# Optimization experiments

Hardware: AMD Instinct MI355X
Metric: run time of the kernel (lower is better)

## Reference

```python
import jax, jax.numpy as jnp
import numpy as np

P = 3            # patch size
PAD = P // 2
K = 8            # candidates kept per pixel
N_ITERS = 5
T = 1.0


def _patch_cost(qpad, kpad, sy, sx, yg, xg):
    # qpad: [C,H+2P,W+2P]; kpad: [C,Hk+2P,Wk+2P]; sy,sx: [N,H,W] int -> cost [N,H,W]
    cost = jnp.zeros(sy.shape, qpad.dtype)
    for dy in range(P):
        for dx in range(P):
            qv = qpad[:, yg + dy, xg + dx]          # [C,H,W]
            kv = kpad[:, sy + dy, sx + dx]          # [C,N,H,W]
            cost = cost + jnp.sum((qv[:, None] - kv) ** 2, axis=0)
    return cost


def _topk_merge(costs, sy, sx, k):
    # keep k smallest costs along candidate axis 0 (sorted ascending)
    neg, idx = jax.lax.top_k(jnp.moveaxis(-costs, 0, -1), k)   # [H,W,k]
    take = lambda a: jnp.moveaxis(jnp.take_along_axis(jnp.moveaxis(a, 0, -1), idx, axis=-1), -1, 0)
    return -jnp.moveaxis(neg, -1, 0), take(sy), take(sx)


def _patchmatch(q, kf, key):
    # q: [C,H,W], kf: [C,Hk,Wk] -> shift maps sy, sx: [K,H,W] int
    C, H, W = q.shape
    Hk, Wk = kf.shape[1], kf.shape[2]
    qpad = jnp.pad(q, ((0, 0), (PAD, PAD), (PAD, PAD)))
    kpad = jnp.pad(kf, ((0, 0), (PAD, PAD), (PAD, PAD)))
    yg, xg = jnp.meshgrid(jnp.arange(H), jnp.arange(W), indexing="ij")
    # random init of K candidates per pixel
    sy = jax.random.randint(jax.random.fold_in(key, 10_000), (K, H, W), 0, Hk)
    sx = jax.random.randint(jax.random.fold_in(key, 10_001), (K, H, W), 0, Wk)
    cost = _patch_cost(qpad, kpad, sy, sx, yg, xg)
    cost, sy, sx = _topk_merge(cost, sy, sx, K)
    r0 = max(Hk, Wk) // 2
    for it in range(N_ITERS):
        by, bx = sy[0], sx[0]
        # parallel propagation from 4 neighbors (shift adjusted by offset)
        cy = [jnp.roll(by, 1, 1), jnp.roll(by, -1, 1),
              jnp.roll(by, 1, 0) + 1, jnp.roll(by, -1, 0) - 1]
        cx = [jnp.roll(bx, 1, 1) + 1, jnp.roll(bx, -1, 1) - 1,
              jnp.roll(bx, 1, 0), jnp.roll(bx, -1, 0)]
        # random search around current best with shrinking radius
        kit = jax.random.fold_in(key, it)
        for s in range(2):
            rad = max(1, r0 >> s)
            dy = jax.random.randint(jax.random.fold_in(kit, 2 * s), (H, W), -rad, rad + 1)
            dx = jax.random.randint(jax.random.fold_in(kit, 2 * s + 1), (H, W), -rad, rad + 1)
            cy.append(by + dy)
            cx.append(bx + dx)
        nsy = jnp.clip(jnp.stack(cy), 0, Hk - 1)
        nsx = jnp.clip(jnp.stack(cx), 0, Wk - 1)
        ncost = _patch_cost(qpad, kpad, nsy, nsx, yg, xg)
        cost, sy, sx = _topk_merge(jnp.concatenate([cost, ncost]),
                                   jnp.concatenate([sy, nsy]),
                                   jnp.concatenate([sx, nsx]), K)
    return sy, sx


def _attention_layer(qi, ki, vi, key):
    # shifts are integer constants (search is non-differentiable in original)
    sy, sx = _patchmatch(jax.lax.stop_gradient(qi), jax.lax.stop_gradient(ki), key)
    H, W = qi.shape[1], qi.shape[2]
    yg, xg = jnp.meshgrid(jnp.arange(H), jnp.arange(W), indexing="ij")
    qpad = jnp.pad(qi, ((0, 0), (PAD, PAD), (PAD, PAD)))
    kpad = jnp.pad(ki, ((0, 0), (PAD, PAD), (PAD, PAD)))
    cost = _patch_cost(qpad, kpad, sy, sx, yg, xg)       # [K,H,W]
    w = jax.nn.softmax(-cost / T, axis=0)                # [K,H,W]
    vg = vi[:, sy, sx]                                   # [Cv,K,H,W]
    return jnp.sum(w[None] * vg, axis=1)                 # [Cv,H,W]


def setup_inputs() -> dict:
    key = jax.random.key(0)
    kq, kk, kv = jax.random.split(key, 3)
    q = jax.random.normal(kq, (2, 32, 256, 256), dtype=jnp.float32)
    k = jax.random.normal(kk, (2, 32, 256, 256), dtype=jnp.float32)
    v = jax.random.normal(kv, (2, 64, 256, 256), dtype=jnp.float32)
    return {"q": q, "k": k, "v": v}


def reference(q, k, v) -> jnp.ndarray:
    B = q.shape[0]
    keys = jax.random.split(jax.random.key(42), B)
    return jax.vmap(_attention_layer)(q, k, v, keys)     # [B,Cv,H,W]
```

## Files before the change

### kernel.cpp

```cpp
#include <hip/hip_runtime.h>
#include <stdint.h>

#define HW 256
#define HWP 258
#define CH 32
#define CVN 64
#define NPIX (HW*HW)
#define KK 8
#define CSTRT (HWP*HWP)


__host__ __device__ __forceinline__ void tf2x32(uint32_t k0, uint32_t k1,
                                                uint32_t x0, uint32_t x1,
                                                uint32_t &o0, uint32_t &o1) {
  const uint32_t ks2 = k0 ^ k1 ^ 0x1BD11BDAu;
  x0 += k0; x1 += k1;
#define TFR(r) x0 += x1; x1 = (x1 << (r)) | (x1 >> (32 - (r))); x1 ^= x0;
  TFR(13) TFR(15) TFR(26) TFR(6)
  x0 += k1;  x1 += ks2 + 1u;
  TFR(17) TFR(29) TFR(16) TFR(24)
  x0 += ks2; x1 += k0 + 2u;
  TFR(13) TFR(15) TFR(26) TFR(6)
  x0 += k0;  x1 += k1 + 3u;
  TFR(17) TFR(29) TFR(16) TFR(24)
  x0 += k1;  x1 += ks2 + 4u;
  TFR(13) TFR(15) TFR(26) TFR(6)
  x0 += ks2; x1 += k0 + 5u;
#undef TFR
  o0 = x0; o1 = x1;
}

__device__ __forceinline__ uint32_t tfbits(uint32_t k0, uint32_t k1, uint32_t idx) {
  uint32_t a, b;
  tf2x32(k0, k1, 0u, idx, a, b);
  return a ^ b;
}

__global__ __launch_bounds__(256) void tpad_k(const float* __restrict__ src,
                                              float* __restrict__ dst) {
  __shared__ float tile[CH][65];
  int t = blockIdx.x;
  int b = t >> 10;
  int p0 = (t & 1023) * 64;
  int tid = threadIdx.x;
  const float* sb = src + (size_t)b * CH * NPIX;
#pragma unroll
  for (int i = 0; i < 8; i++) {
    int idx = i * 256 + tid;
    int c = idx >> 6, px = idx & 63;
    tile[c][px] = sb[c * NPIX + p0 + px];
  }
  __syncthreads();
  float* db = dst + (size_t)b * CSTRT * CH;
#pragma unroll
  for (int i = 0; i < 8; i++) {
    int idx = i * 256 + tid;
    int px = idx >> 5, c = idx & 31;
    int p = p0 + px;
    int y = p >> 8, x = p & 255;
    db[((size_t)(y + 1) * HWP + (x + 1)) * CH + c] = tile[c][px];
  }
}

__global__ __launch_bounds__(256) void vtr_k(const float* __restrict__ v,
                                             float* __restrict__ vp) {
  __shared__ float tile[CVN][65];
  int t = blockIdx.x;
  int b = t >> 10;
  int p0 = (t & 1023) * 64;
  int tid = threadIdx.x;
  const float* sb = v + (size_t)b * CVN * NPIX;
#pragma unroll
  for (int i = 0; i < 16; i++) {
    int idx = i * 256 + tid;
    int c = idx >> 6, px = idx & 63;
    tile[c][px] = sb[c * NPIX + p0 + px];
  }
  __syncthreads();
  float* db = vp + (size_t)b * NPIX * CVN;
#pragma unroll
  for (int i = 0; i < 16; i++) {
    int idx = i * 256 + tid;
    int px = idx >> 6, c = idx & 63;
    db[(size_t)(p0 + px) * CVN + c] = tile[c][px];
  }
}

__device__ __forceinline__ float cost_full(const float* __restrict__ qt,
                                           int py, int px,
                                           const float* __restrict__ kb2,
                                           int sy, int sx) {
#pragma clang fp contract(off)
  float S[3][3];
  const float* kb = kb2 + ((size_t)sy * HWP + sx) * CH;
#pragma unroll
  for (int dy = 0; dy < 3; dy++) {
#pragma unroll
    for (int dx = 0; dx < 3; dx++) {
      int row = py + dy, col = px + dx;
      const float* qrow = &qt[(row * 18 + col) * 32];
      int rot = 4 * ((row * 3 + col) & 7);
      const float* kr = kb + (dy * HWP + dx) * CH;
      float4 kv[8], qv[8];
#pragma unroll
      for (int i = 0; i < 8; i++) kv[i] = ((const float4*)kr)[i];
#pragma unroll
      for (int i = 0; i < 8; i++)
        qv[i] = *(const float4*)(&qrow[(i * 4 + rot) & 31]);
      float s = 0.f;
#pragma unroll
      for (int i = 0; i < 8; i++) {
        float d;
        d = qv[i].x - kv[i].x; s = s + d * d;
        d = qv[i].y - kv[i].y; s = s + d * d;
        d = qv[i].z - kv[i].z; s = s + d * d;
        d = qv[i].w - kv[i].w; s = s + d * d;
      }
      S[dy][dx] = s;
    }
  }
  float cost = 0.f;
#pragma unroll
  for (int dy = 0; dy < 3; dy++)
#pragma unroll
    for (int dx = 0; dx < 3; dx++) cost = cost + S[dy][dx];
  return cost;
}

__device__ __forceinline__ float cost_ch(const float* __restrict__ qt,
                                         int py, int px,
                                         const float* __restrict__ kb2,
                                         int sy, int sx) {
#pragma clang fp contract(off)
  float S[3][3];
#pragma unroll
  for (int dy = 0; dy < 3; dy++)
#pragma unroll
    for (int dx = 0; dx < 3; dx++) S[dy][dx] = 0.f;
  const float* kb = kb2 + ((size_t)sy * HWP + sx) * CH;
#pragma unroll 2
  for (int ch = 0; ch < CH; ch += 4) {
#pragma unroll
    for (int dy = 0; dy < 3; dy++) {
#pragma unroll
      for (int dx = 0; dx < 3; dx++) {
        int row = py + dy, col = px + dx;
        const float4 qv = *(const float4*)(&qt[(row * 18 + col) * 32 +
                                              ((ch + 4 * ((row * 3 + col) & 7)) & 31)]);
        const float4 kv = *(const float4*)(kb + (dy * HWP + dx) * CH + ch);
        float d;
        d = qv.x - kv.x; S[dy][dx] = S[dy][dx] + d * d;
        d = qv.y - kv.y; S[dy][dx] = S[dy][dx] + d * d;
        d = qv.z - kv.z; S[dy][dx] = S[dy][dx] + d * d;
        d = qv.w - kv.w; S[dy][dx] = S[dy][dx] + d * d;
      }
    }
  }
  float cost = 0.f;
#pragma unroll
  for (int dy = 0; dy < 3; dy++)
#pragma unroll
    for (int dx = 0; dx < 3; dx++) cost = cost + S[dy][dx];
  return cost;
}

__device__ __forceinline__ void load_qtile16(const float* __restrict__ qpb,
                                             float* __restrict__ qt,
                                             int ty, int tx, int tid) {
  for (int i = tid; i < 18 * 18 * 8; i += 256) {
    int c4 = i & 7;
    int col = (i >> 3) % 18;
    int row = (i >> 3) / 18;
    float4 v = *(const float4*)(qpb + ((size_t)(ty + row) * HWP + (tx + col)) * CH + c4 * 4);
    *(float4*)(&qt[(row * 18 + col) * 32 +
                   ((c4 * 4 + 4 * ((row * 3 + col) & 7)) & 31)]) = v;
  }
}

__global__ __launch_bounds__(256) void init11_k(
    const float* __restrict__ qp2, const float* __restrict__ kp2,
    float* __restrict__ cO, int* __restrict__ sO,
    uint4 ikA, uint4 ikB) {
  __shared__ float qt[18 * 18 * 32];
  __shared__ uint32_t ent[2048];
  __shared__ float lc[256][9];
  __shared__ int bcnt[8], bstart[9], boff[8];
  int tid = threadIdx.x;
  int grp = blockIdx.x;
  int b = grp >> 8;
  int tin = grp & 255;
  int ty = (tin >> 4) * 16, tx = (tin & 15) * 16;
  const float* qpb = qp2 + (size_t)b * CSTRT * CH;
  const float* kpb = kp2 + (size_t)b * CSTRT * CH;
  load_qtile16(qpb, qt, ty, tx, tid);
  if (tid < 8) bcnt[tid] = 0;
  __syncthreads();

  int py = tid >> 4, px = tid & 15;
  int p = ((ty + py) << 8) | (tx + px);
  uint4 K = b ? ikB : ikA;
  int scand[KK];
#pragma unroll
  for (int j = 0; j < KK; j++) {
    uint32_t cand = (uint32_t)(j * NPIX + p);
    int sy = (int)(tfbits(K.x, K.y, cand) & 255u);
    int sx = (int)(tfbits(K.z, K.w, cand) & 255u);
    scand[j] = (sy << 8) | sx;
    atomicAdd(&bcnt[sy >> 5], 1);
  }
  __syncthreads();
  if (tid == 0) {
    int s = 0;
#pragma unroll
    for (int i = 0; i < 8; i++) { bstart[i] = s; boff[i] = s; s += bcnt[i]; }
    bstart[8] = s;
  }
  __syncthreads();
#pragma unroll
  for (int j = 0; j < KK; j++) {
    int pos = atomicAdd(&boff[scand[j] >> 13], 1);
    ent[pos] = ((uint32_t)scand[j] << 11) | ((uint32_t)tid << 3) | (uint32_t)j;
  }
  __syncthreads();

  for (int band = 0; band < 8; band++) {
    int s = bstart[band], t = bstart[band + 1];
    for (int i = s + tid; i < t; i += 256) {
      uint32_t en = ent[i];
      int j = en & 7, owner = (en >> 3) & 255;
      int ps = en >> 11;
      lc[owner][j] = cost_full(qt, owner >> 4, owner & 15, kpb, ps >> 8, ps & 255);
    }
    __syncthreads();
  }

  float c8[KK];
  int s8[KK];
#pragma unroll
  for (int jj = 0; jj < KK; jj++) { c8[jj] = lc[tid][jj]; s8[jj] = scand[jj]; }
#pragma unroll
  for (int ph = 0; ph < KK; ph++) {
#pragma unroll
    for (int i = (ph & 1); i + 1 < KK; i += 2) {
      if (c8[i] > c8[i + 1]) {
        float tc = c8[i]; c8[i] = c8[i + 1]; c8[i + 1] = tc;
        int ts = s8[i]; s8[i] = s8[i + 1]; s8[i + 1] = ts;
      }
    }
  }
  int base = b * KK * NPIX;
#pragma unroll
  for (int jj = 0; jj < KK; jj++) {
    cO[base + jj * NPIX + p] = c8[jj];
    sO[base + jj * NPIX + p] = s8[jj];
  }
}

__device__ __forceinline__ void prop_cand(const int* __restrict__ sI, int base,
                                          int y, int x, int c, int &nsy, int &nsx) {
  int np;
  if (c == 0)      np = (y << 8) | ((x + HW - 1) & (HW - 1));
  else if (c == 1) np = (y << 8) | ((x + 1) & (HW - 1));
  else if (c == 2) np = (((y + HW - 1) & (HW - 1)) << 8) | x;
  else             np = (((y + 1) & (HW - 1)) << 8) | x;
  int sv = sI[base + np];
  if (c == 0)      { nsy = sv >> 8;       nsx = (sv & 255) + 1; }
  else if (c == 1) { nsy = sv >> 8;       nsx = (sv & 255) - 1; }
  else if (c == 2) { nsy = (sv >> 8) + 1; nsx = sv & 255; }
  else             { nsy = (sv >> 8) - 1; nsx = sv & 255; }
}

__device__ __forceinline__ int rand_off(uint4 K, uint32_t p, int s) {
  uint32_t hi = tfbits(K.x, K.y, p), lo = tfbits(K.z, K.w, p);
  return (s == 0) ? (int)(((hi % 257u) + (lo % 257u)) % 257u) - 128
                  : (int)((((hi % 129u) * 16u) + (lo % 129u)) % 129u) - 64;
}

__global__ __launch_bounds__(256) void iter13_k(
    const float* __restrict__ qp2, const float* __restrict__ kp2,
    const float* __restrict__ cI, const int* __restrict__ sI,
    float* __restrict__ cO, int* __restrict__ sO,
    uint4 A0y, uint4 A0x, uint4 A1y, uint4 A1x,
    uint4 B0y, uint4 B0x, uint4 B1y, uint4 B1x) {
  __shared__ float qt[18 * 18 * 32];
  __shared__ uint32_t ent[1536];
  __shared__ float lc[256][7];
  __shared__ int bcnt[4], bstart[5], boff[4];
  int tid = threadIdx.x;
  int bid = blockIdx.x;
  int b = ((bid & 7) >= 4) ? 1 : 0;
  int tin = ((bid >> 3) << 2) | (bid & 3);
  int ty = (tin >> 4) * 16, tx = (tin & 15) * 16;
  int base = b * KK * NPIX;
  const float* qpb = qp2 + (size_t)b * CSTRT * CH;
  const float* kpb = kp2 + (size_t)b * CSTRT * CH;
  load_qtile16(qpb, qt, ty, tx, tid);
  if (tid < 4) bcnt[tid] = 0;
  __syncthreads();

  int py = tid >> 4, px = tid & 15;
  int y = ty + py, x = tx + px;
  int p = (y << 8) | x;
  int pcur[KK];
#pragma unroll
  for (int jj = 0; jj < KK; jj++) pcur[jj] = sI[base + jj * NPIX + p];

  int scand[6];
  int dupj[6];
#pragma unroll
  for (int j = 0; j < 6; j++) {
    int nsy, nsx;
    if (j < 4) {
      prop_cand(sI, base, y, x, j, nsy, nsx);
    } else {
      int by = pcur[0] >> 8, bx = pcur[0] & 255;
      int s = j - 4;
      uint4 KY = b ? (s ? B1y : B0y) : (s ? A1y : A0y);
      uint4 KX = b ? (s ? B1x : B0x) : (s ? A1x : A0x);
      nsy = by + rand_off(KY, (uint32_t)p, s);
      nsx = bx + rand_off(KX, (uint32_t)p, s);
    }
    nsy = min(max(nsy, 0), HW - 1);
    nsx = min(max(nsx, 0), HW - 1);
    int ps = (nsy << 8) | nsx;
    scand[j] = ps;
    int d = -1;
#pragma unroll
    for (int jj = 0; jj < KK; jj++)
      if (d < 0 && pcur[jj] == ps) d = jj;
    dupj[j] = d;
    if (d < 0) atomicAdd(&bcnt[nsy >> 6], 1);
  }
  __syncthreads();
  if (tid == 0) {
    int s = 0;
#pragma unroll
    for (int i = 0; i < 4; i++) { bstart[i] = s; boff[i] = s; s += bcnt[i]; }
    bstart[4] = s;
  }
  __syncthreads();
#pragma unroll
  for (int j = 0; j < 6; j++) {
    if (dupj[j] < 0) {
      int pos = atomicAdd(&boff[scand[j] >> 14], 1);
      ent[pos] = ((uint32_t)scand[j] << 11) | ((uint32_t)tid << 3) | (uint32_t)j;
    }
  }
  __syncthreads();

  for (int band = 0; band < 4; band++) {
    int s = bstart[band], t = bstart[band + 1];
    for (int i = s + tid; i < t; i += 256) {
      uint32_t en = ent[i];
      int j = en & 7, owner = (en >> 3) & 255;
      int ps = en >> 11;
      lc[owner][j] = cost_ch(qt, owner >> 4, owner & 15, kpb, ps >> 8, ps & 255);
    }
    __syncthreads();
  }

  float c14[KK + 6];
  int s14[KK + 6];
#pragma unroll
  for (int jj = 0; jj < KK; jj++) {
    c14[jj] = cI[base + jj * NPIX + p];
    s14[jj] = pcur[jj];
  }
#pragma unroll
  for (int j = 0; j < 6; j++) {
    int d = dupj[j];
    c14[KK + j] = (d >= 0) ? c14[d] : lc[tid][j];
    s14[KK + j] = scand[j];
  }
#pragma unroll
  for (int ph = 0; ph < 14; ph++) {
#pragma unroll
    for (int i = (ph & 1); i + 1 < 14; i += 2) {
      if (c14[i] > c14[i + 1]) {
        float tc = c14[i]; c14[i] = c14[i + 1]; c14[i + 1] = tc;
        int ts = s14[i]; s14[i] = s14[i + 1]; s14[i + 1] = ts;
      }
    }
  }
#pragma unroll
  for (int jj = 0; jj < KK; jj++) {
    cO[base + jj * NPIX + p] = c14[jj];
    sO[base + jj * NPIX + p] = s14[jj];
  }
}

__global__ __launch_bounds__(256) void attn5_k(
    const float* __restrict__ vp, const float* __restrict__ cI,
    const int* __restrict__ sI, float* __restrict__ out) {
  int g = threadIdx.x >> 6;
  int pl = threadIdx.x & 63;
  int gpix = blockIdx.x * 64 + pl;
  int b = gpix >> 16, p = gpix & 0xFFFF;
  int base = b * KK * NPIX;
  float c[KK];
  int off[KK];
#pragma unroll
  for (int j = 0; j < KK; j++) {
    c[j] = cI[base + j * NPIX + p];
    off[j] = sI[base + j * NPIX + p];
  }
  float m = c[0];
  float w[KK];
  float Z = 0.f;
#pragma unroll
  for (int j = 0; j < KK; j++) { w[j] = expf(m - c[j]); Z = Z + w[j]; }
#pragma unroll
  for (int j = 0; j < KK; j++) w[j] = w[j] / Z;
  int bd[KK];
#pragma unroll
  for (int j = 0; j < KK; j++) bd[j] = off[j] >> 12;
  const float* vb = vp + (size_t)b * NPIX * CVN + g * 16;
  float acc[16];
#pragma unroll
  for (int i = 0; i < 16; i++) acc[i] = 0.f;
  for (int band = 0; band < 16; band++) {
#pragma unroll
    for (int j = 0; j < KK; j++) {
      if (bd[j] == band) {
        const float4* vr = (const float4*)(vb + (size_t)off[j] * CVN);
#pragma unroll
        for (int t = 0; t < 4; t++) {
          float4 vv = vr[t];
          acc[t * 4 + 0] = acc[t * 4 + 0] + w[j] * vv.x;
          acc[t * 4 + 1] = acc[t * 4 + 1] + w[j] * vv.y;
          acc[t * 4 + 2] = acc[t * 4 + 2] + w[j] * vv.z;
          acc[t * 4 + 3] = acc[t * 4 + 3] + w[j] * vv.w;
        }
      }
    }
  }
  float* ob = out + (size_t)b * CVN * NPIX;
#pragma unroll
  for (int i = 0; i < 16; i++) ob[(size_t)(g * 16 + i) * NPIX + p] = acc[i];
}

extern "C" void kernel_launch(void* const* d_in, const int* in_sizes, int n_in,
                              void* d_out, int out_size, void* d_ws, size_t ws_size,
                              hipStream_t stream) {
  const float* q = (const float*)d_in[0];
  const float* k = (const float*)d_in[1];
  const float* v = (const float*)d_in[2];
  float* out = (float*)d_out;

  uint32_t kA0, kA1, kB0, kB1;
  tf2x32(0u, 42u, 0u, 0u, kA0, kA1);
  tf2x32(0u, 42u, 0u, 1u, kB0, kB1);

  uint4 ikA, ikB;
  {
    uint32_t f0, f1;
    tf2x32(kA0, kA1, 0u, 10000u, f0, f1); tf2x32(f0, f1, 0u, 1u, ikA.x, ikA.y);
    tf2x32(kA0, kA1, 0u, 10001u, f0, f1); tf2x32(f0, f1, 0u, 1u, ikA.z, ikA.w);
    tf2x32(kB0, kB1, 0u, 10000u, f0, f1); tf2x32(f0, f1, 0u, 1u, ikB.x, ikB.y);
    tf2x32(kB0, kB1, 0u, 10001u, f0, f1); tf2x32(f0, f1, 0u, 1u, ikB.z, ikB.w);
  }

  const size_t szPad = (size_t)2 * CSTRT * CH;
  const size_t szCS  = (size_t)2 * KK * NPIX;
  float* qp2 = (float*)d_ws;
  float* kp2 = qp2 + szPad;
  float* cA = kp2 + szPad;
  float* cB = cA + szCS;
  int* sA = (int*)(cB + szCS);
  int* sB = sA + szCS;
  float* vp = (float*)(sB + szCS);

  hipMemsetAsync(qp2, 0, szPad * sizeof(float), stream);
  hipMemsetAsync(kp2, 0, szPad * sizeof(float), stream);
  tpad_k<<<2048, 256, 0, stream>>>(q, qp2);
  tpad_k<<<2048, 256, 0, stream>>>(k, kp2);
  vtr_k<<<2048, 256, 0, stream>>>(v, vp);

  init11_k<<<512, 256, 0, stream>>>(qp2, kp2, cA, sA, ikA, ikB);

  float* ci = cA; int* si = sA;
  float* co = cB; int* so = sB;
  for (int it = 0; it < 5; ++it) {
    uint4 ky[2][2], kx[2][2];
    for (int bb = 0; bb < 2; bb++) {
      uint32_t kk0 = bb ? kB0 : kA0, kk1 = bb ? kB1 : kA1;
      uint32_t kit0, kit1;
      tf2x32(kk0, kk1, 0u, (uint32_t)it, kit0, kit1);
      for (int s = 0; s < 2; s++) {
        uint32_t f0, f1, h0, h1, l0, l1;
        tf2x32(kit0, kit1, 0u, (uint32_t)(2 * s), f0, f1);
        tf2x32(f0, f1, 0u, 0u, h0, h1);
        tf2x32(f0, f1, 0u, 1u, l0, l1);
        ky[bb][s] = make_uint4(h0, h1, l0, l1);
        tf2x32(kit0, kit1, 0u, (uint32_t)(2 * s + 1), f0, f1);
        tf2x32(f0, f1, 0u, 0u, h0, h1);
        tf2x32(f0, f1, 0u, 1u, l0, l1);
        kx[bb][s] = make_uint4(h0, h1, l0, l1);
      }
    }
    iter13_k<<<512, 256, 0, stream>>>(qp2, kp2, ci, si, co, so,
                                      ky[0][0], kx[0][0], ky[0][1], kx[0][1],
                                      ky[1][0], kx[1][0], ky[1][1], kx[1][1]);
    float* tc = ci; ci = co; co = tc;
    int* ts = si; si = so; so = ts;
  }
  attn5_k<<<2048, 256, 0, stream>>>(vp, ci, si, out);
}
```

Baseline: 1.025 ms.

## Split iteration kernel into generate, evaluate and merge kernels

The fused per-iteration kernel is split into three launches. The first generates candidates and bucket lists into global scratch, the second evaluates patch costs with the shared q tile, and the third performs the sort-merge per pixel. The scratch arrays reuse the value-transpose buffer, so the value transpose now runs after the search. The intent is to lower shared-memory and register pressure per kernel and raise occupancy during cost evaluation. The cost is extra launches and global round-trips for candidates, duplicates and costs, and cost evaluation switches from cost_ch to cost_full.

```diff
diff --git a/kernel.cpp b/kernel.cpp
--- a/kernel.cpp
+++ b/kernel.cpp
@@ -127,43 +127,6 @@
   return cost;
 }
 
-__device__ __forceinline__ float cost_ch(const float* __restrict__ qt,
-                                         int py, int px,
-                                         const float* __restrict__ kb2,
-                                         int sy, int sx) {
-#pragma clang fp contract(off)
-  float S[3][3];
-#pragma unroll
-  for (int dy = 0; dy < 3; dy++)
-#pragma unroll
-    for (int dx = 0; dx < 3; dx++) S[dy][dx] = 0.f;
-  const float* kb = kb2 + ((size_t)sy * HWP + sx) * CH;
-#pragma unroll 2
-  for (int ch = 0; ch < CH; ch += 4) {
-#pragma unroll
-    for (int dy = 0; dy < 3; dy++) {
-#pragma unroll
-      for (int dx = 0; dx < 3; dx++) {
-        int row = py + dy, col = px + dx;
-        const float4 qv = *(const float4*)(&qt[(row * 18 + col) * 32 +
-                                              ((ch + 4 * ((row * 3 + col) & 7)) & 31)]);
-        const float4 kv = *(const float4*)(kb + (dy * HWP + dx) * CH + ch);
-        float d;
-        d = qv.x - kv.x; S[dy][dx] = S[dy][dx] + d * d;
-        d = qv.y - kv.y; S[dy][dx] = S[dy][dx] + d * d;
-        d = qv.z - kv.z; S[dy][dx] = S[dy][dx] + d * d;
-        d = qv.w - kv.w; S[dy][dx] = S[dy][dx] + d * d;
-      }
-    }
-  }
-  float cost = 0.f;
-#pragma unroll
-  for (int dy = 0; dy < 3; dy++)
-#pragma unroll
-    for (int dx = 0; dx < 3; dx++) cost = cost + S[dy][dx];
-  return cost;
-}
-
 __device__ __forceinline__ void load_qtile16(const float* __restrict__ qpb,
                                              float* __restrict__ qt,
                                              int ty, int tx, int tid) {
@@ -276,15 +239,13 @@
                   : (int)((((hi % 129u) * 16u) + (lo % 129u)) % 129u) - 64;
 }
 
-__global__ __launch_bounds__(256) void iter13_k(
-    const float* __restrict__ qp2, const float* __restrict__ kp2,
-    const float* __restrict__ cI, const int* __restrict__ sI,
-    float* __restrict__ cO, int* __restrict__ sO,
+__global__ __launch_bounds__(256) void gen_k(
+    const int* __restrict__ sI,
+    int* __restrict__ scandG, int* __restrict__ dupjG,
+    uint32_t* __restrict__ entG, int* __restrict__ bstG,
     uint4 A0y, uint4 A0x, uint4 A1y, uint4 A1x,
     uint4 B0y, uint4 B0x, uint4 B1y, uint4 B1x) {
-  __shared__ float qt[18 * 18 * 32];
   __shared__ uint32_t ent[1536];
-  __shared__ float lc[256][7];
   __shared__ int bcnt[4], bstart[5], boff[4];
   int tid = threadIdx.x;
   int bid = blockIdx.x;
@@ -292,12 +253,8 @@
   int tin = ((bid >> 3) << 2) | (bid & 3);
   int ty = (tin >> 4) * 16, tx = (tin & 15) * 16;
   int base = b * KK * NPIX;
-  const float* qpb = qp2 + (size_t)b * CSTRT * CH;
-  const float* kpb = kp2 + (size_t)b * CSTRT * CH;
-  load_qtile16(qpb, qt, ty, tx, tid);
   if (tid < 4) bcnt[tid] = 0;
   __syncthreads();
-
   int py = tid >> 4, px = tid & 15;
   int y = ty + py, x = tx + px;
   int p = (y << 8) | x;
@@ -347,30 +304,67 @@
     }
   }
   __syncthreads();
-
+  int gp6 = (b * NPIX + p) * 6;
+#pragma unroll
+  for (int j = 0; j < 6; j++) {
+    scandG[gp6 + j] = scand[j];
+    dupjG[gp6 + j] = dupj[j];
+  }
+  int total = bstart[4];
+  for (int i = tid; i < total; i += 256) entG[bid * 1536 + i] = ent[i];
+  if (tid < 5) bstG[bid * 8 + tid] = bstart[tid];
+}
+
+__global__ __launch_bounds__(256) void eval_k(
+    const float* __restrict__ qp2, const float* __restrict__ kp2,
+    const uint32_t* __restrict__ entG, const int* __restrict__ bstG,
+    float* __restrict__ lcG) {
+  __shared__ float qt[18 * 18 * 32];
+  int tid = threadIdx.x;
+  int bid = blockIdx.x;
+  int b = ((bid & 7) >= 4) ? 1 : 0;
+  int tin = ((bid >> 3) << 2) | (bid & 3);
+  int ty = (tin >> 4) * 16, tx = (tin & 15) * 16;
+  const float* qpb = qp2 + (size_t)b * CSTRT * CH;
+  const float* kpb = kp2 + (size_t)b * CSTRT * CH;
+  load_qtile16(qpb, qt, ty, tx, tid);
+  __syncthreads();
+  const uint32_t* ent = entG + bid * 1536;
   for (int band = 0; band < 4; band++) {
-    int s = bstart[band], t = bstart[band + 1];
+    int s = bstG[bid * 8 + band], t = bstG[bid * 8 + band + 1];
     for (int i = s + tid; i < t; i += 256) {
       uint32_t en = ent[i];
       int j = en & 7, owner = (en >> 3) & 255;
       int ps = en >> 11;
-      lc[owner][j] = cost_ch(qt, owner >> 4, owner & 15, kpb, ps >> 8, ps & 255);
+      float c = cost_full(qt, owner >> 4, owner & 15, kpb, ps >> 8, ps & 255);
+      int p = ((ty + (owner >> 4)) << 8) | (tx + (owner & 15));
+      lcG[(size_t)(b * NPIX + p) * 6 + j] = c;
     }
     __syncthreads();
   }
-
+}
+
+__global__ __launch_bounds__(256) void merge_k(
+    const float* __restrict__ cI, const int* __restrict__ sI,
+    const int* __restrict__ scandG, const int* __restrict__ dupjG,
+    const float* __restrict__ lcG,
+    float* __restrict__ cO, int* __restrict__ sO) {
+  int gpix = blockIdx.x * 256 + threadIdx.x;
+  int b = gpix >> 16, p = gpix & 0xFFFF;
+  int base = b * KK * NPIX;
   float c14[KK + 6];
   int s14[KK + 6];
 #pragma unroll
   for (int jj = 0; jj < KK; jj++) {
     c14[jj] = cI[base + jj * NPIX + p];
-    s14[jj] = pcur[jj];
-  }
+    s14[jj] = sI[base + jj * NPIX + p];
+  }
+  int gp6 = gpix * 6;
 #pragma unroll
   for (int j = 0; j < 6; j++) {
-    int d = dupj[j];
-    c14[KK + j] = (d >= 0) ? c14[d] : lc[tid][j];
-    s14[KK + j] = scand[j];
+    int d = dupjG[gp6 + j];
+    c14[KK + j] = (d >= 0) ? c14[d] : lcG[gp6 + j];
+    s14[KK + j] = scandG[gp6 + j];
   }
 #pragma unroll
   for (int ph = 0; ph < 14; ph++) {
@@ -470,11 +464,16 @@
   int* sB = sA + szCS;
   float* vp = (float*)(sB + szCS);
 
+  uint32_t* entG = (uint32_t*)vp;
+  int* bstG = (int*)(entG + 512 * 1536);
+  int* scandG = bstG + 512 * 8;
+  int* dupjG = scandG + (size_t)2 * NPIX * 6;
+  float* lcG = (float*)(dupjG + (size_t)2 * NPIX * 6);
+
   hipMemsetAsync(qp2, 0, szPad * sizeof(float), stream);
   hipMemsetAsync(kp2, 0, szPad * sizeof(float), stream);
   tpad_k<<<2048, 256, 0, stream>>>(q, qp2);
   tpad_k<<<2048, 256, 0, stream>>>(k, kp2);
-  vtr_k<<<2048, 256, 0, stream>>>(v, vp);
 
   init11_k<<<512, 256, 0, stream>>>(qp2, kp2, cA, sA, ikA, ikB);
 
@@ -498,11 +497,15 @@
         kx[bb][s] = make_uint4(h0, h1, l0, l1);
       }
     }
-    iter13_k<<<512, 256, 0, stream>>>(qp2, kp2, ci, si, co, so,
-                                      ky[0][0], kx[0][0], ky[0][1], kx[0][1],
-                                      ky[1][0], kx[1][0], ky[1][1], kx[1][1]);
+    gen_k<<<512, 256, 0, stream>>>(si, scandG, dupjG, entG, bstG,
+                                   ky[0][0], kx[0][0], ky[0][1], kx[0][1],
+                                   ky[1][0], kx[1][0], ky[1][1], kx[1][1]);
+    eval_k<<<512, 256, 0, stream>>>(qp2, kp2, entG, bstG, lcG);
+    merge_k<<<512, 256, 0, stream>>>(ci, si, scandG, dupjG, lcG, co, so);
     float* tc = ci; ci = co; co = tc;
     int* ts = si; si = so; so = ts;
   }
+
+  vtr_k<<<2048, 256, 0, stream>>>(v, vp);
   attn5_k<<<2048, 256, 0, stream>>>(vp, ci, si, out);
 }
```

Result: slower. 1.058 ms (+3.2%).
